# Kernel tuning notes

Hardware: AMD Instinct MI355X
Metric: run time of the kernel (lower is better)

The kernel has to match this reference:

```python
import jax, jax.numpy as jnp
import numpy as np

N, C, W, H = 16, 64, 512, 512
RED, OUT_W = 64, 128
BN_EPS = 1e-5


def setup_inputs() -> dict:
    key = jax.random.key(0)
    ks = jax.random.split(key, 5)
    x = jax.random.normal(ks[0], (N, C, W, H), dtype=jnp.float32)
    w1 = jax.random.normal(ks[1], (RED, W), dtype=jnp.float32) * (1.0 / np.sqrt(W))
    b1 = jax.random.normal(ks[2], (RED,), dtype=jnp.float32) * 0.01
    gamma = jnp.ones((RED,), dtype=jnp.float32)
    beta = jnp.zeros((RED,), dtype=jnp.float32)
    w2 = jax.random.normal(ks[3], (W, RED), dtype=jnp.float32) * (1.0 / np.sqrt(RED))
    b2 = jax.random.normal(ks[4], (W,), dtype=jnp.float32) * 0.01
    return {"x": x, "w1": w1, "b1": b1, "gamma": gamma, "beta": beta, "w2": w2, "b2": b2}


def reference(x, w1, b1, gamma, beta, w2, b2):
    # attention_dim == 2: permute(0,2,1,3) -> [N,W,C,H]; AdaptiveMaxPool2d((1,1))
    # over (C,H) == global max over axes (1,3) of original x -> [N, W]
    pooled = jnp.max(x, axis=(1, 3))                       # [N, W]
    # Linear(W -> RED)
    h = pooled @ w1.T + b1                                 # [N, RED]
    # BatchNorm1d in training mode: batch stats (biased variance)
    mu = jnp.mean(h, axis=0)
    var = jnp.mean((h - mu) ** 2, axis=0)
    h = gamma * (h - mu) * jax.lax.rsqrt(var + BN_EPS) + beta
    h = jax.nn.relu(h)
    # Linear(RED -> W) + softmax over width
    att = jax.nn.softmax(h @ w2.T + b2, axis=1)            # [N, W]
    # topk over width, then sort selected indices ascending
    _, idx = jax.lax.top_k(att, OUT_W)                     # [N, OUT_W]
    idx = jnp.sort(idx, axis=1)
    # batched gather along width axis: x[i, :, idx[i], :]
    return jnp.take_along_axis(x, idx[:, None, :, None], axis=2)  # [N, C, OUT_W, H]
```

## Files before the change

kernel.cpp:

```cpp
#include <hip/hip_runtime.h>
#include <cstdint>
#include <math.h>

#define Nn   16
#define Cc   64
#define Ww   512
#define Hh   512
#define RED  64
#define OUTW 128

__global__ void pool_kernel(const float* __restrict__ x, float* __restrict__ pooled) {
    const int b = blockIdx.x;
    const int n = b >> 9;
    const int w = b & 511;
    const float* base = x + ((size_t)n * Cc * Ww + w) * Hh;
    const int tid = threadIdx.x;
    float m = -INFINITY;
    #pragma unroll 4
    for (int i = tid; i < Cc * (Hh / 4); i += 256) {
        const int c = i >> 7;
        const int f = i & 127;
        const float4 v = *reinterpret_cast<const float4*>(base + (size_t)c * (Ww * Hh) + f * 4);
        m = fmaxf(fmaxf(fmaxf(m, v.x), fmaxf(v.y, v.z)), v.w);
    }
    #pragma unroll
    for (int off = 32; off > 0; off >>= 1)
        m = fmaxf(m, __shfl_down(m, off, 64));
    __shared__ float red[4];
    if ((tid & 63) == 0) red[tid >> 6] = m;
    __syncthreads();
    if (tid == 0)
        pooled[b] = fmaxf(fmaxf(red[0], red[1]), fmaxf(red[2], red[3]));
}

__global__ void __launch_bounds__(512) mlp_topk_kernel(
    const float* __restrict__ pooled,
    const float* __restrict__ w1,
    const float* __restrict__ b1,
    const float* __restrict__ gamma,
    const float* __restrict__ beta,
    const float* __restrict__ w2,
    const float* __restrict__ b2,
    int* __restrict__ idx_out)
{
    const int row = blockIdx.x;
    const int tid = threadIdx.x;

    __shared__ float pooled_t[Ww][Nn + 1];
    __shared__ float hbn_t[RED][Nn + 1];
    __shared__ float mu_s[RED], is_s[RED];
    __shared__ float logits_row[Ww];
    __shared__ unsigned long long sel_mask[Ww / 64];

    for (int i = tid; i < Nn * Ww; i += 512) {
        const int n = i >> 9, k = i & 511;
        pooled_t[k][n] = pooled[i];
    }
    __syncthreads();

    float hv[2];
    int hn[2], hr[2];
    #pragma unroll
    for (int e = 0; e < 2; ++e) {
        const int item = e * 512 + tid;
        const int n = item & 15, r = item >> 4;
        hn[e] = n; hr[e] = r;
        float acc = b1[r];
        for (int k = 0; k < Ww; ++k)
            acc += pooled_t[k][n] * w1[r * Ww + k];
        hv[e] = acc;
    }
    #pragma unroll
    for (int e = 0; e < 2; ++e) hbn_t[hr[e]][hn[e]] = hv[e];
    __syncthreads();

    if (tid < RED) {
        float s = 0.f, s2 = 0.f;
        #pragma unroll
        for (int n = 0; n < Nn; ++n) { const float v = hbn_t[tid][n]; s += v; s2 += v * v; }
        const float mu  = s  * (1.f / Nn);
        const float var = s2 * (1.f / Nn) - mu * mu;
        mu_s[tid] = mu;
        is_s[tid] = 1.f / sqrtf(var + 1e-5f);
    }
    __syncthreads();

    #pragma unroll
    for (int e = 0; e < 2; ++e) {
        const int r = hr[e], n = hn[e];
        const float v = gamma[r] * (hv[e] - mu_s[r]) * is_s[r] + beta[r];
        hbn_t[r][n] = fmaxf(v, 0.f);
    }
    __syncthreads();

    {
        const int w = tid;
        float acc = b2[w];
        #pragma unroll
        for (int r = 0; r < RED; ++r)
            acc += hbn_t[r][row] * w2[w * RED + r];
        logits_row[w] = acc;
    }
    __syncthreads();

    {
        const int w = tid;
        const float v = logits_row[w];
        int rank = 0;
        for (int ww = 0; ww < Ww; ++ww) {
            const float u = logits_row[ww];
            rank += (u > v || (u == v && ww < w)) ? 1 : 0;
        }
        const bool sel = (rank < OUTW);
        const unsigned long long m = __ballot(sel);
        if ((tid & 63) == 0) sel_mask[tid >> 6] = m;
        __syncthreads();
        if (sel) {
            int pos = 0;
            #pragma unroll
            for (int bb = 0; bb < (Ww / 64); ++bb)
                if (bb < (w >> 6)) pos += __popcll(sel_mask[bb]);
            pos += __popcll(sel_mask[w >> 6] & ((1ULL << (w & 63)) - 1ULL));
            idx_out[row * OUTW + pos] = w;
        }
    }
}

__global__ void gather_kernel(const float* __restrict__ x,
                              const int* __restrict__ idx,
                              float* __restrict__ out) {
    const int b = blockIdx.x;
    const int n = b >> 7;
    const int j = b & 127;
    const int w = idx[b];
    const float* src = x   + ((size_t)n * Cc * Ww   + w) * Hh;
    float*       dst = out + ((size_t)n * Cc * OUTW + j) * Hh;
    const int tid = threadIdx.x;
    #pragma unroll 4
    for (int i = tid; i < Cc * (Hh / 4); i += 256) {
        const int c = i >> 7;
        const int f = i & 127;
        const float4 v = *reinterpret_cast<const float4*>(src + (size_t)c * (Ww * Hh) + f * 4);
        *reinterpret_cast<float4*>(dst + (size_t)c * (OUTW * Hh) + f * 4) = v;
    }
}

extern "C" void kernel_launch(void* const* d_in, const int* in_sizes, int n_in,
                              void* d_out, int out_size, void* d_ws, size_t ws_size,
                              hipStream_t stream) {
    const float* x     = (const float*)d_in[0];
    const float* w1    = (const float*)d_in[1];
    const float* b1    = (const float*)d_in[2];
    const float* gamma = (const float*)d_in[3];
    const float* beta  = (const float*)d_in[4];
    const float* w2    = (const float*)d_in[5];
    const float* b2    = (const float*)d_in[6];
    float* out = (float*)d_out;

    float* pooled = (float*)d_ws;
    int*   idx    = (int*)((char*)d_ws + Nn * Ww * sizeof(float));

    pool_kernel<<<Nn * Ww, 256, 0, stream>>>(x, pooled);
    mlp_topk_kernel<<<Nn, 512, 0, stream>>>(pooled, w1, b1, gamma, beta, w2, b2, idx);
    gather_kernel<<<Nn * OUTW, 256, 0, stream>>>(x, idx, out);
}
```

Baseline: 344.4 us.

## Reorganize pool and gather kernels to walk contiguous (n,c) planes

The pool kernel now gives each block one contiguous (n,c) plane of x. Each wavefront reduces whole rows and combines partial maxima across channels with atomicMax on order-preserving encoded floats, which needs an extra init kernel to zero the buffer. The gather kernel likewise gives each block one (n,c) plane, with the indices staged in shared memory. The aim is long contiguous streaming reads instead of 2KB strided chunks spread across channels. The cost is one extra launch and 64-way atomic contention per pooled element.

```diff
diff --git a/kernel.cpp b/kernel.cpp
--- a/kernel.cpp
+++ b/kernel.cpp
@@ -9,32 +9,51 @@
 #define RED  64
 #define OUTW 128
 
-__global__ void pool_kernel(const float* __restrict__ x, float* __restrict__ pooled) {
+__device__ __forceinline__ unsigned enc_f32(float f) {
+    unsigned b = __float_as_uint(f);
+    return (b & 0x80000000u) ? ~b : (b | 0x80000000u);
+}
+__device__ __forceinline__ float dec_f32(unsigned u) {
+    unsigned b = (u & 0x80000000u) ? (u & 0x7FFFFFFFu) : ~u;
+    return __uint_as_float(b);
+}
+
+__global__ void init_kernel(unsigned* __restrict__ pu) {
+    pu[blockIdx.x * 256 + threadIdx.x] = 0u;
+}
+
+__global__ void __launch_bounds__(256) pool_kernel(const float* __restrict__ x,
+                                                   unsigned* __restrict__ pu) {
     const int b = blockIdx.x;
-    const int n = b >> 9;
-    const int w = b & 511;
-    const float* base = x + ((size_t)n * Cc * Ww + w) * Hh;
-    const int tid = threadIdx.x;
-    float m = -INFINITY;
-    #pragma unroll 4
-    for (int i = tid; i < Cc * (Hh / 4); i += 256) {
-        const int c = i >> 7;
-        const int f = i & 127;
-        const float4 v = *reinterpret_cast<const float4*>(base + (size_t)c * (Ww * Hh) + f * 4);
-        m = fmaxf(fmaxf(fmaxf(m, v.x), fmaxf(v.y, v.z)), v.w);
+    const int n = b >> 6;
+    const float* plane = x + (size_t)b * (Ww * Hh);
+    const int wv   = threadIdx.x >> 6;
+    const int lane = threadIdx.x & 63;
+    const int rbase = wv * 128;
+
+    #pragma unroll 2
+    for (int it = 0; it < 64; ++it) {
+        const int r0 = rbase + it * 2;
+        const float4* p0 = reinterpret_cast<const float4*>(plane + (size_t)r0 * Hh);
+        const float4* p1 = reinterpret_cast<const float4*>(plane + (size_t)(r0 + 1) * Hh);
+        const float4 a0 = p0[lane], b0 = p0[lane + 64];
+        const float4 a1 = p1[lane], b1 = p1[lane + 64];
+        float m0 = fmaxf(fmaxf(fmaxf(a0.x, a0.y), fmaxf(a0.z, a0.w)),
+                         fmaxf(fmaxf(b0.x, b0.y), fmaxf(b0.z, b0.w)));
+        float m1 = fmaxf(fmaxf(fmaxf(a1.x, a1.y), fmaxf(a1.z, a1.w)),
+                         fmaxf(fmaxf(b1.x, b1.y), fmaxf(b1.z, b1.w)));
+        #pragma unroll
+        for (int off = 1; off < 64; off <<= 1) {
+            m0 = fmaxf(m0, __shfl_xor(m0, off, 64));
+            m1 = fmaxf(m1, __shfl_xor(m1, off, 64));
+        }
+        if (lane == 0) atomicMax(&pu[n * Ww + r0],     enc_f32(m0));
+        if (lane == 1) atomicMax(&pu[n * Ww + r0 + 1], enc_f32(m1));
     }
-    #pragma unroll
-    for (int off = 32; off > 0; off >>= 1)
-        m = fmaxf(m, __shfl_down(m, off, 64));
-    __shared__ float red[4];
-    if ((tid & 63) == 0) red[tid >> 6] = m;
-    __syncthreads();
-    if (tid == 0)
-        pooled[b] = fmaxf(fmaxf(red[0], red[1]), fmaxf(red[2], red[3]));
 }
 
 __global__ void __launch_bounds__(512) mlp_topk_kernel(
-    const float* __restrict__ pooled,
+    const unsigned* __restrict__ pu,
     const float* __restrict__ w1,
     const float* __restrict__ b1,
     const float* __restrict__ gamma,
@@ -54,7 +73,7 @@
 
     for (int i = tid; i < Nn * Ww; i += 512) {
         const int n = i >> 9, k = i & 511;
-        pooled_t[k][n] = pooled[i];
+        pooled_t[k][n] = dec_f32(pu[i]);
     }
     __syncthreads();
 
@@ -126,22 +145,23 @@
     }
 }
 
-__global__ void gather_kernel(const float* __restrict__ x,
-                              const int* __restrict__ idx,
-                              float* __restrict__ out) {
+__global__ void __launch_bounds__(256) gather_kernel(const float* __restrict__ x,
+                                                     const int* __restrict__ idx,
+                                                     float* __restrict__ out) {
     const int b = blockIdx.x;
-    const int n = b >> 7;
-    const int j = b & 127;
-    const int w = idx[b];
-    const float* src = x   + ((size_t)n * Cc * Ww   + w) * Hh;
-    float*       dst = out + ((size_t)n * Cc * OUTW + j) * Hh;
+    const int n = b >> 6;
     const int tid = threadIdx.x;
+    __shared__ int sidx[OUTW];
+    if (tid < OUTW) sidx[tid] = idx[n * OUTW + tid];
+    __syncthreads();
+    const float* src = x   + (size_t)b * (Ww * Hh);
+    float*       dst = out + (size_t)b * (OUTW * Hh);
     #pragma unroll 4
-    for (int i = tid; i < Cc * (Hh / 4); i += 256) {
-        const int c = i >> 7;
+    for (int i = tid; i < OUTW * (Hh / 4); i += 256) {
+        const int j = i >> 7;
         const int f = i & 127;
-        const float4 v = *reinterpret_cast<const float4*>(src + (size_t)c * (Ww * Hh) + f * 4);
-        *reinterpret_cast<float4*>(dst + (size_t)c * (OUTW * Hh) + f * 4) = v;
+        const float4 v = *reinterpret_cast<const float4*>(src + (size_t)sidx[j] * Hh + f * 4);
+        *reinterpret_cast<float4*>(dst + (size_t)j * Hh + f * 4) = v;
     }
 }
 
@@ -157,10 +177,11 @@
     const float* b2    = (const float*)d_in[6];
     float* out = (float*)d_out;
 
-    float* pooled = (float*)d_ws;
-    int*   idx    = (int*)((char*)d_ws + Nn * Ww * sizeof(float));
+    unsigned* pu  = (unsigned*)d_ws;
+    int*      idx = (int*)((char*)d_ws + Nn * Ww * sizeof(unsigned));
 
-    pool_kernel<<<Nn * Ww, 256, 0, stream>>>(x, pooled);
-    mlp_topk_kernel<<<Nn, 512, 0, stream>>>(pooled, w1, b1, gamma, beta, w2, b2, idx);
-    gather_kernel<<<Nn * OUTW, 256, 0, stream>>>(x, idx, out);
+    init_kernel<<<(Nn * Ww) / 256, 256, 0, stream>>>(pu);
+    pool_kernel<<<Nn * Cc, 256, 0, stream>>>(x, pu);
+    mlp_topk_kernel<<<Nn, 512, 0, stream>>>(pu, w1, b1, gamma, beta, w2, b2, idx);
+    gather_kernel<<<Nn * Cc, 256, 0, stream>>>(x, idx, out);
 }
```

New measurement: 370.1 us. 7.5% more time.

## Remap pool to one wavefront per width row and gather per channel

Applied to the files above, without the earlier changes.

The pool kernel now assigns one 64-lane wavefront to each width position, so each block covers 4 widths. Each lane loads two float4s per channel and keeps eight independent max accumulators, and the final reduction is a single wave xor-shuffle with no shared memory or barrier. The gather kernel now runs one block per (n, c) pair, stages that sample's 128 indices in shared memory, and copies contiguous rows into a contiguous output plane. The aim is more memory-level parallelism and coalesced writes, at the cost of fewer blocks in both kernels and a block barrier in the gather.

```diff
diff --git a/kernel.cpp b/kernel.cpp
--- a/kernel.cpp
+++ b/kernel.cpp
@@ -9,28 +9,34 @@
 #define RED  64
 #define OUTW 128
 
-__global__ void pool_kernel(const float* __restrict__ x, float* __restrict__ pooled) {
+__global__ void __launch_bounds__(256) pool_kernel(const float* __restrict__ x,
+                                                   float* __restrict__ pooled) {
     const int b = blockIdx.x;
-    const int n = b >> 9;
-    const int w = b & 511;
-    const float* base = x + ((size_t)n * Cc * Ww + w) * Hh;
-    const int tid = threadIdx.x;
-    float m = -INFINITY;
+    const int n = b >> 7;
+    const int q = b & 127;
+    const int r = threadIdx.x >> 6;
+    const int lane = threadIdx.x & 63;
+    const int w = q * 4 + r;
+    const float* base = x + ((size_t)n * Cc * Ww + w) * Hh + lane * 8;
+
+    float m0 = -INFINITY, m1 = -INFINITY, m2 = -INFINITY, m3 = -INFINITY;
+    float m4 = -INFINITY, m5 = -INFINITY, m6 = -INFINITY, m7 = -INFINITY;
     #pragma unroll 4
-    for (int i = tid; i < Cc * (Hh / 4); i += 256) {
-        const int c = i >> 7;
-        const int f = i & 127;
-        const float4 v = *reinterpret_cast<const float4*>(base + (size_t)c * (Ww * Hh) + f * 4);
-        m = fmaxf(fmaxf(fmaxf(m, v.x), fmaxf(v.y, v.z)), v.w);
+    for (int c = 0; c < Cc; ++c) {
+        const float* p = base + (size_t)c * (Ww * Hh);
+        const float4 v0 = *reinterpret_cast<const float4*>(p);
+        const float4 v1 = *reinterpret_cast<const float4*>(p + 4);
+        m0 = fmaxf(m0, v0.x); m1 = fmaxf(m1, v0.y);
+        m2 = fmaxf(m2, v0.z); m3 = fmaxf(m3, v0.w);
+        m4 = fmaxf(m4, v1.x); m5 = fmaxf(m5, v1.y);
+        m6 = fmaxf(m6, v1.z); m7 = fmaxf(m7, v1.w);
     }
+    float m = fmaxf(fmaxf(fmaxf(m0, m1), fmaxf(m2, m3)),
+                    fmaxf(fmaxf(m4, m5), fmaxf(m6, m7)));
     #pragma unroll
-    for (int off = 32; off > 0; off >>= 1)
-        m = fmaxf(m, __shfl_down(m, off, 64));
-    __shared__ float red[4];
-    if ((tid & 63) == 0) red[tid >> 6] = m;
-    __syncthreads();
-    if (tid == 0)
-        pooled[b] = fmaxf(fmaxf(red[0], red[1]), fmaxf(red[2], red[3]));
+    for (int off = 1; off < 64; off <<= 1)
+        m = fmaxf(m, __shfl_xor(m, off, 64));
+    if (lane == 0) pooled[n * Ww + w] = m;
 }
 
 __global__ void __launch_bounds__(512) mlp_topk_kernel(
@@ -126,22 +132,23 @@
     }
 }
 
-__global__ void gather_kernel(const float* __restrict__ x,
-                              const int* __restrict__ idx,
-                              float* __restrict__ out) {
+__global__ void __launch_bounds__(256) gather_kernel(const float* __restrict__ x,
+                                                     const int* __restrict__ idx,
+                                                     float* __restrict__ out) {
     const int b = blockIdx.x;
-    const int n = b >> 7;
-    const int j = b & 127;
-    const int w = idx[b];
-    const float* src = x   + ((size_t)n * Cc * Ww   + w) * Hh;
-    float*       dst = out + ((size_t)n * Cc * OUTW + j) * Hh;
+    const int n = b >> 6;
     const int tid = threadIdx.x;
+    __shared__ int sidx[OUTW];
+    if (tid < OUTW) sidx[tid] = idx[n * OUTW + tid];
+    __syncthreads();
+    const float* src = x   + (size_t)b * (Ww * Hh);
+    float*       dst = out + (size_t)b * (OUTW * Hh);
     #pragma unroll 4
-    for (int i = tid; i < Cc * (Hh / 4); i += 256) {
-        const int c = i >> 7;
+    for (int i = tid; i < OUTW * (Hh / 4); i += 256) {
+        const int j = i >> 7;
         const int f = i & 127;
-        const float4 v = *reinterpret_cast<const float4*>(src + (size_t)c * (Ww * Hh) + f * 4);
-        *reinterpret_cast<float4*>(dst + (size_t)c * (OUTW * Hh) + f * 4) = v;
+        const float4 v = *reinterpret_cast<const float4*>(src + (size_t)sidx[j] * Hh + f * 4);
+        *reinterpret_cast<float4*>(dst + (size_t)j * Hh + f * 4) = v;
     }
 }
 
@@ -160,7 +167,7 @@
     float* pooled = (float*)d_ws;
     int*   idx    = (int*)((char*)d_ws + Nn * Ww * sizeof(float));
 
-    pool_kernel<<<Nn * Ww, 256, 0, stream>>>(x, pooled);
+    pool_kernel<<<Nn * (Ww / 4), 256, 0, stream>>>(x, pooled);
     mlp_topk_kernel<<<Nn, 512, 0, stream>>>(pooled, w1, b1, gamma, beta, w2, b2, idx);
-    gather_kernel<<<Nn * OUTW, 256, 0, stream>>>(x, idx, out);
+    gather_kernel<<<Nn * Cc, 256, 0, stream>>>(x, idx, out);
 }
```

After: 345.0 us. Within noise of the previous version (+0.2%).
